# Optimization experiments

Hardware: AMD Instinct MI355X
Metric: run time of the kernel (lower is better)

Reference implementation:

```python
import jax, jax.numpy as jnp
import numpy as np

EMB = 1024
HEADS = 16
HEAD_DIM = EMB // HEADS
B, S = 2, 2048
FF = 4 * EMB
EPS = 1e-5


def setup_inputs() -> dict:
    key = jax.random.key(0)
    ks = jax.random.split(key, 16)
    sc = 0.02
    return {
        "x": jax.random.normal(ks[0], (B, S, EMB), dtype=jnp.float32),
        "ln1_scale": jnp.ones((EMB,), jnp.float32),
        "ln1_shift": jnp.zeros((EMB,), jnp.float32),
        "ln2_scale": jnp.ones((EMB,), jnp.float32),
        "ln2_shift": jnp.zeros((EMB,), jnp.float32),
        "wq": jax.random.normal(ks[1], (EMB, EMB), jnp.float32) * sc,
        "bq": jnp.zeros((EMB,), jnp.float32),
        "wk": jax.random.normal(ks[2], (EMB, EMB), jnp.float32) * sc,
        "bk": jnp.zeros((EMB,), jnp.float32),
        "wv": jax.random.normal(ks[3], (EMB, EMB), jnp.float32) * sc,
        "bv": jnp.zeros((EMB,), jnp.float32),
        "wo": jax.random.normal(ks[4], (EMB, EMB), jnp.float32) * sc,
        "bo": jnp.zeros((EMB,), jnp.float32),
        "w_fc": jax.random.normal(ks[5], (EMB, FF), jnp.float32) * sc,
        "b_fc": jnp.zeros((FF,), jnp.float32),
        "w_proj": jax.random.normal(ks[6], (FF, EMB), jnp.float32) * sc,
        "b_proj": jnp.zeros((EMB,), jnp.float32),
    }


def _layernorm(x, scale, shift):
    # Faithful to source: unbiased std (ddof=1) and eps added to std, not var.
    mean = jnp.mean(x, axis=-1, keepdims=True)
    std = jnp.std(x, axis=-1, keepdims=True, ddof=1)
    return scale * ((x - mean) / (std + EPS)) + shift


def _gelu(x):
    c = jnp.sqrt(jnp.asarray(2.0 / np.pi, x.dtype))
    return 0.5 * x * (1.0 + jnp.tanh(c * (x + 0.044715 * x * x * x)))


def _attention(x, wq, bq, wk, bk, wv, bv, wo, bo):
    b, s, _ = x.shape
    q = (x @ wq + bq).reshape(b, s, HEADS, HEAD_DIM).transpose(0, 2, 1, 3)
    k = (x @ wk + bk).reshape(b, s, HEADS, HEAD_DIM).transpose(0, 2, 1, 3)
    v = (x @ wv + bv).reshape(b, s, HEADS, HEAD_DIM).transpose(0, 2, 1, 3)
    scores = jnp.einsum("bhqd,bhkd->bhqk", q, k)  # [B,H,S,S]
    causal = jnp.triu(jnp.ones((s, s), bool), k=1)
    scores = jnp.where(causal, -jnp.inf, scores)
    attn = jax.nn.softmax(scores / jnp.sqrt(jnp.asarray(HEAD_DIM, x.dtype)), axis=-1)
    ctx = jnp.einsum("bhqk,bhkd->bhqd", attn, v)
    ctx = ctx.transpose(0, 2, 1, 3).reshape(b, s, EMB)
    return ctx @ wo + bo


def reference(x, ln1_scale, ln1_shift, ln2_scale, ln2_shift,
              wq, bq, wk, bk, wv, bv, wo, bo,
              w_fc, b_fc, w_proj, b_proj):
    h = x + _attention(_layernorm(x, ln1_scale, ln1_shift), wq, bq, wk, bk, wv, bv, wo, bo)
    m = _layernorm(h, ln2_scale, ln2_shift)
    m = _gelu(m @ w_fc + b_fc) @ w_proj + b_proj
    return h + m
```

## Files before the change

kernel.cpp:

```cpp
#include <hip/hip_runtime.h>
#include <hip/hip_bf16.h>

typedef float f32x4 __attribute__((ext_vector_type(4)));
typedef __bf16 bf16x8 __attribute__((ext_vector_type(8)));

#define EMB 1024
#define FFD 4096
#define NHEAD 16
#define HD 64
#define SEQ 2048
#define MROWS 4096

__device__ __forceinline__ unsigned short f2bf(float f) {
    unsigned int x = __builtin_bit_cast(unsigned int, f);
    x += 0x7fffu + ((x >> 16) & 1u);
    return (unsigned short)(x >> 16);
}

__device__ __forceinline__ unsigned int pack2bf(float a, float b) {
    return (unsigned int)f2bf(a) | ((unsigned int)f2bf(b) << 16);
}

__device__ __forceinline__ f32x4 mfma16(bf16x8 a, bf16x8 b, f32x4 c) {
    return __builtin_amdgcn_mfma_f32_16x16x32_bf16(a, b, c, 0, 0, 0);
}

__device__ __forceinline__ bf16x8 scale8(bf16x8 v, float s) {
    bf16x8 o;
#pragma unroll
    for (int i = 0; i < 8; ++i) o[i] = (__bf16)((float)v[i] * s);
    return o;
}

__device__ __forceinline__ float gelu_f(float x) {
    float u = 0.7978845608028654f * (x + 0.044715f * x * x * x);
    float e = __expf(2.0f * u);
    float th = 1.0f - 2.0f / (e + 1.0f);
    return 0.5f * x * (1.0f + th);
}

__device__ __forceinline__ void xcd_remap(int& bx, int& by) {
    const int nbx = gridDim.x;
    int id = blockIdx.x + nbx * blockIdx.y;
    int xcd = id & 7, i = id >> 3;
    by = (i / nbx) * 8 + xcd;
    bx = i % nbx;
}

template <int EPI>
__global__ __launch_bounds__(256) void gemm_bt(
    const unsigned short* __restrict__ A, const unsigned short* __restrict__ Bt,
    const float* __restrict__ bias,
    void* __restrict__ outp, int M, int N, int K)
{
    __shared__ unsigned short As[2][128 * 32];
    __shared__ unsigned short Bs[2][128 * 32];
    const int tid  = threadIdx.x;
    const int lane = tid & 63;
    const int wid  = tid >> 6;
    int bx, by; xcd_remap(bx, by);
    const int brow = by << 7;
    const int bcol = bx << 7;
    const int wr = wid >> 1, wc = wid & 1;

    f32x4 acc[4][4];
    const f32x4 zero = {0.f, 0.f, 0.f, 0.f};
#pragma unroll
    for (int m = 0; m < 4; ++m)
#pragma unroll
        for (int n = 0; n < 4; ++n) acc[m][n] = zero;

    const int nk = K >> 5;

    auto stage = [&](int buf, int k0) {
#pragma unroll
        for (int c = 0; c < 2; ++c) {
            int idx = (wid << 10) + (c << 9) + (lane << 3);
            int row = idx >> 5;
            int c8s = (idx >> 3) & 3;
            int c8g = c8s ^ ((row >> 1) & 3);
            const unsigned short* ga = A  + (size_t)(brow + row) * K + k0 + (c8g << 3);
            const unsigned short* gb = Bt + (size_t)(bcol + row) * K + k0 + (c8g << 3);
            __builtin_amdgcn_global_load_lds(
                (const __attribute__((address_space(1))) unsigned int*)ga,
                (__attribute__((address_space(3))) unsigned int*)&As[buf][idx], 16, 0, 0);
            __builtin_amdgcn_global_load_lds(
                (const __attribute__((address_space(1))) unsigned int*)gb,
                (__attribute__((address_space(3))) unsigned int*)&Bs[buf][idx], 16, 0, 0);
        }
    };

    stage(0, 0);
    for (int kt = 0; kt < nk; ++kt) {
        __syncthreads();
        if (kt + 1 < nk) stage((kt + 1) & 1, (kt + 1) << 5);
        const unsigned short* as = As[kt & 1];
        const unsigned short* bs = Bs[kt & 1];
        const int kg = lane >> 4;
        bf16x8 afr[4], bfr[4];
#pragma unroll
        for (int m = 0; m < 4; ++m) {
            int row = (wr << 6) + (m << 4) + (lane & 15);
            int c8  = kg ^ ((row >> 1) & 3);
            afr[m] = *(const bf16x8*)&as[(row << 5) + (c8 << 3)];
        }
#pragma unroll
        for (int n = 0; n < 4; ++n) {
            int row = (wc << 6) + (n << 4) + (lane & 15);
            int c8  = kg ^ ((row >> 1) & 3);
            bfr[n] = *(const bf16x8*)&bs[(row << 5) + (c8 << 3)];
        }
#pragma unroll
        for (int m = 0; m < 4; ++m)
#pragma unroll
            for (int n = 0; n < 4; ++n)
                acc[m][n] = mfma16(afr[m], bfr[n], acc[m][n]);
        __syncthreads();
    }

#pragma unroll
    for (int m = 0; m < 4; ++m) {
#pragma unroll
        for (int n = 0; n < 4; ++n) {
            const int col = bcol + (wc << 6) + (n << 4) + (lane & 15);
            const float bv = bias[col];
#pragma unroll
            for (int r = 0; r < 4; ++r) {
                const int row = brow + (wr << 6) + (m << 4) + ((lane >> 4) << 2) + r;
                float v = acc[m][n][r] + bv;
                if (EPI == 1) v = gelu_f(v);
                ((unsigned short*)outp)[(size_t)row * N + col] = f2bf(v);
            }
        }
    }
}

__global__ __launch_bounds__(256) void gemm_bt_n64(
    const unsigned short* __restrict__ A, const unsigned short* __restrict__ Bt,
    const float* __restrict__ bias, const float* __restrict__ resid,
    float* __restrict__ outp, int M, int N, int K)
{
    __shared__ unsigned short As[2][128 * 64];
    __shared__ unsigned short Bs[2][64 * 64];
    const int tid  = threadIdx.x;
    const int lane = tid & 63;
    const int wid  = tid >> 6;
    int bx, by; xcd_remap(bx, by);
    const int brow = by << 7;
    const int bcol = bx << 6;

    f32x4 acc[2][4];
    const f32x4 zero = {0.f, 0.f, 0.f, 0.f};
#pragma unroll
    for (int m = 0; m < 2; ++m)
#pragma unroll
        for (int n = 0; n < 4; ++n) acc[m][n] = zero;

    const int nk = K >> 6;

    auto stage = [&](int buf, int k0) {
#pragma unroll
        for (int c = 0; c < 4; ++c) {
            int idx = (c << 11) + (tid << 3);
            int row = idx >> 6;
            int c8g = ((idx >> 3) & 7) ^ (row & 7);
            const unsigned short* ga = A + (size_t)(brow + row) * K + k0 + (c8g << 3);
            __builtin_amdgcn_global_load_lds(
                (const __attribute__((address_space(1))) unsigned int*)ga,
                (__attribute__((address_space(3))) unsigned int*)&As[buf][idx], 16, 0, 0);
        }
#pragma unroll
        for (int c = 0; c < 2; ++c) {
            int idx = (c << 11) + (tid << 3);
            int row = idx >> 6;
            int c8g = ((idx >> 3) & 7) ^ (row & 7);
            const unsigned short* gb = Bt + (size_t)(bcol + row) * K + k0 + (c8g << 3);
            __builtin_amdgcn_global_load_lds(
                (const __attribute__((address_space(1))) unsigned int*)gb,
                (__attribute__((address_space(3))) unsigned int*)&Bs[buf][idx], 16, 0, 0);
        }
    };

    stage(0, 0);
    for (int kt = 0; kt < nk; ++kt) {
        __syncthreads();
        if (kt + 1 < nk) stage((kt + 1) & 1, (kt + 1) << 6);
        const unsigned short* as = As[kt & 1];
        const unsigned short* bs = Bs[kt & 1];
        const int kg = lane >> 4;
#pragma unroll
        for (int f = 0; f < 2; ++f) {
            bf16x8 afr[2], bfr[4];
#pragma unroll
            for (int m = 0; m < 2; ++m) {
                int row = (wid << 5) + (m << 4) + (lane & 15);
                int c8  = ((f << 2) + kg) ^ (row & 7);
                afr[m] = *(const bf16x8*)&as[(row << 6) + (c8 << 3)];
            }
#pragma unroll
            for (int n = 0; n < 4; ++n) {
                int row = (n << 4) + (lane & 15);
                int c8  = ((f << 2) + kg) ^ (row & 7);
                bfr[n] = *(const bf16x8*)&bs[(row << 6) + (c8 << 3)];
            }
#pragma unroll
            for (int m = 0; m < 2; ++m)
#pragma unroll
                for (int n = 0; n < 4; ++n)
                    acc[m][n] = mfma16(afr[m], bfr[n], acc[m][n]);
        }
        __syncthreads();
    }

#pragma unroll
    for (int m = 0; m < 2; ++m)
#pragma unroll
        for (int n = 0; n < 4; ++n) {
            const int col = bcol + (n << 4) + (lane & 15);
            const float bv = bias[col];
#pragma unroll
            for (int r = 0; r < 4; ++r) {
                const int row = brow + (wid << 5) + (m << 4) + ((lane >> 4) << 2) + r;
                outp[(size_t)row * N + col] =
                    acc[m][n][r] + bv + resid[(size_t)row * N + col];
            }
        }
}

__global__ __launch_bounds__(256) void layernorm_k(
    const float* __restrict__ x, const float* __restrict__ sc,
    const float* __restrict__ sh, unsigned short* __restrict__ outp)
{
    const int row = blockIdx.x;
    const int tid = threadIdx.x;
    const float4 v = ((const float4*)(x + (size_t)row * EMB))[tid];
    float s  = v.x + v.y + v.z + v.w;
    float ss = v.x * v.x + v.y * v.y + v.z * v.z + v.w * v.w;
#pragma unroll
    for (int o = 32; o > 0; o >>= 1) {
        s  += __shfl_down(s, o);
        ss += __shfl_down(ss, o);
    }
    __shared__ float red[8];
    if ((tid & 63) == 0) { red[tid >> 6] = s; red[(tid >> 6) + 4] = ss; }
    __syncthreads();
    s  = red[0] + red[1] + red[2] + red[3];
    ss = red[4] + red[5] + red[6] + red[7];
    const float mean = s * (1.0f / EMB);
    const float var  = (ss - s * mean) * (1.0f / (EMB - 1));
    const float inv  = 1.0f / (sqrtf(var) + 1e-5f);
    const int c = tid << 2;
    ushort4 o4;
    o4.x = f2bf((v.x - mean) * inv * sc[c + 0] + sh[c + 0]);
    o4.y = f2bf((v.y - mean) * inv * sc[c + 1] + sh[c + 1]);
    o4.z = f2bf((v.z - mean) * inv * sc[c + 2] + sh[c + 2]);
    o4.w = f2bf((v.w - mean) * inv * sc[c + 3] + sh[c + 3]);
    ((ushort4*)(outp + (size_t)row * EMB))[tid] = o4;
}

__global__ __launch_bounds__(256) void vtrans_k(
    const unsigned short* __restrict__ qkv, unsigned short* __restrict__ vt)
{
    __shared__ unsigned short T[64 * 64];
    const int tid = threadIdx.x;
    const int st = blockIdx.x, h = blockIdx.y, b = blockIdx.z;
    const size_t rowbase = (size_t)b * SEQ;
    const unsigned short* vsrc = qkv + (rowbase + (st << 6)) * 3072 + 2 * EMB + h * 64;
#pragma unroll
    for (int it = 0; it < 2; ++it) {
        const int s  = (it << 5) + (tid >> 3);
        const int d8 = tid & 7;
        uint4 w = *(const uint4*)(vsrc + (size_t)s * 3072 + (d8 << 3));
        *(uint4*)&T[(s << 6) + ((d8 ^ (s & 7)) << 3)] = w;
    }
    __syncthreads();
    unsigned short* vdst = vt + ((size_t)(b * NHEAD + h) << 6) * SEQ + (st << 6);
#pragma unroll
    for (int it = 0; it < 2; ++it) {
        const int d  = (it << 5) + (tid >> 3);
        const int s8 = tid & 7;
        unsigned short o8[8];
#pragma unroll
        for (int j = 0; j < 8; ++j) {
            const int s = (s8 << 3) + j;
            o8[j] = T[(s << 6) + (((d >> 3) ^ (s & 7)) << 3) + (d & 7)];
        }
        *(uint4*)(vdst + (size_t)d * SEQ + (s8 << 3)) = *(const uint4*)o8;
    }
}

__global__ __launch_bounds__(256) void attn_k(
    const unsigned short* __restrict__ qkv, const unsigned short* __restrict__ vt,
    unsigned short* __restrict__ ctx)
{
    __shared__ unsigned short Ks[2][64 * 64];
    __shared__ unsigned short Vts[2][64 * 64];
    __shared__ unsigned short Ps[4][16 * 64];
    const int tid  = threadIdx.x;
    const int lane = tid & 63;
    const int wid  = tid >> 6;
    const int q    = lane & 15;
    const int lg   = lane >> 4;

    const int id = blockIdx.x;
    const int xcd = id & 7, i = id >> 3;
    const int grp = ((i >> 4) << 3) + xcd;
    const int pairi = i & 15;
    const int h = grp & 15;
    const int b = grp >> 4;

    const size_t rowbase = (size_t)b * SEQ;
    const unsigned short* kbase = qkv + rowbase * 3072 + EMB + h * 64;
    const unsigned short* vbase = vt + ((size_t)(b * NHEAD + h) << 6) * SEQ;

    auto stage = [&](int buf, int t) {
#pragma unroll
        for (int c = 0; c < 2; ++c) {
            const int idx = (wid << 10) + (c << 9) + (lane << 3);
            {
                const int kv  = idx >> 6;
                const int d8s = ((idx >> 3) & 7) ^ (kv & 7);
                const unsigned short* g = kbase + (size_t)((t << 6) + kv) * 3072 + (d8s << 3);
                __builtin_amdgcn_global_load_lds(
                    (const __attribute__((address_space(1))) unsigned int*)g,
                    (__attribute__((address_space(3))) unsigned int*)&Ks[buf][idx], 16, 0, 0);
            }
            {
                const int d   = idx >> 6;
                const int s8s = ((idx >> 3) & 7) ^ (d & 7);
                const unsigned short* g = vbase + (size_t)d * SEQ + (t << 6) + (s8s << 3);
                __builtin_amdgcn_global_load_lds(
                    (const __attribute__((address_space(1))) unsigned int*)g,
                    (__attribute__((address_space(3))) unsigned int*)&Vts[buf][idx], 16, 0, 0);
            }
        }
    };

    const f32x4 zero = {0.f, 0.f, 0.f, 0.f};
    const float QSC = 0.18033688011112042f;

#pragma unroll 1
    for (int pass = 0; pass < 2; ++pass) {
        const int qt = pass ? (31 - pairi) : pairi;
        const int qrow0 = (qt << 6) + (wid << 4);
        const int qglob = qrow0 + q;

        bf16x8 qf[2];
        {
            const unsigned short* qp = qkv + (rowbase + qglob) * 3072 + h * 64;
            qf[0] = scale8(*(const bf16x8*)&qp[(lg << 3)], QSC);
            qf[1] = scale8(*(const bf16x8*)&qp[32 + (lg << 3)], QSC);
        }

        f32x4 accd[4];
#pragma unroll
        for (int dg = 0; dg < 4; ++dg) accd[dg] = zero;
        float mrow = -__builtin_inff();
        float lrow = 0.f;

        stage(0, 0);
#pragma unroll 1
        for (int t = 0; t <= qt; ++t) {
            __syncthreads();
            if (t < qt) stage((t + 1) & 1, t + 1);
            const unsigned short* ks = Ks[t & 1];
            const unsigned short* vs = Vts[t & 1];

            f32x4 sg[4];
#pragma unroll
            for (int g = 0; g < 4; ++g) {
                f32x4 sv = zero;
#pragma unroll
                for (int f = 0; f < 2; ++f) {
                    const int krow = (g << 4) + q;
                    const int cb   = (f << 5) + (lg << 3);
                    bf16x8 kf = *(const bf16x8*)&ks[(krow << 6) + (cb ^ ((krow & 7) << 3))];
                    sv = mfma16(kf, qf[f], sv);
                }
                sg[g] = sv;
            }
            if (t == qt) {
#pragma unroll
                for (int g = 0; g < 4; ++g) {
#pragma unroll
                    for (int r = 0; r < 4; ++r) {
                        const int kvg = (t << 6) + (g << 4) + (lg << 2) + r;
                        if (kvg > qglob) sg[g][r] = -__builtin_inff();
                    }
                }
            }

            float mx = sg[0][0];
#pragma unroll
            for (int g = 0; g < 4; ++g)
#pragma unroll
                for (int r = 0; r < 4; ++r) mx = fmaxf(mx, sg[g][r]);
            mx = fmaxf(mx, __shfl_xor(mx, 16));
            mx = fmaxf(mx, __shfl_xor(mx, 32));
            if (__any(mx > mrow + 8.0f)) {
                const float mn = fmaxf(mrow, mx);
                const float so = exp2f(mrow - mn);
                mrow = mn;
                lrow *= so;
#pragma unroll
                for (int dg = 0; dg < 4; ++dg) accd[dg] *= so;
            }
            float rs = 0.f;
#pragma unroll
            for (int g = 0; g < 4; ++g)
#pragma unroll
                for (int r = 0; r < 4; ++r) {
                    const float pv = exp2f(sg[g][r] - mrow);
                    sg[g][r] = pv;
                    rs += pv;
                }
            rs += __shfl_xor(rs, 16);
            rs += __shfl_xor(rs, 32);
            lrow += rs;

#pragma unroll
            for (int g = 0; g < 4; ++g) {
                uint2 w;
                w.x = pack2bf(sg[g][0], sg[g][1]);
                w.y = pack2bf(sg[g][2], sg[g][3]);
                const int e = ((g << 4) + (lg << 2)) ^ ((q & 7) << 3);
                *(uint2*)&Ps[wid][(q << 6) + e] = w;
            }

            bf16x8 pa[2];
#pragma unroll
            for (int f = 0; f < 2; ++f) {
                const int e = ((f << 5) + (lg << 3)) ^ ((q & 7) << 3);
                pa[f] = *(const bf16x8*)&Ps[wid][(q << 6) + e];
            }
#pragma unroll
            for (int dg = 0; dg < 4; ++dg) {
#pragma unroll
                for (int f = 0; f < 2; ++f) {
                    const int vrow = (dg << 4) + q;
                    const int cb   = (f << 5) + (lg << 3);
                    bf16x8 vb = *(const bf16x8*)&vs[(vrow << 6) + (cb ^ ((vrow & 7) << 3))];
                    accd[dg] = mfma16(vb, pa[f], accd[dg]);
                }
            }
        }

        const float inv = 1.0f / lrow;
        unsigned short* cp = ctx + (rowbase + qglob) * EMB + h * 64 + (lg << 2);
#pragma unroll
        for (int dg = 0; dg < 4; ++dg) {
            uint2 w;
            w.x = pack2bf(accd[dg][0] * inv, accd[dg][1] * inv);
            w.y = pack2bf(accd[dg][2] * inv, accd[dg][3] * inv);
            *(uint2*)(cp + (dg << 4)) = w;
        }
        __syncthreads();
    }
}

__global__ __launch_bounds__(256) void transpose_cvt(
    const float* __restrict__ W, unsigned short* __restrict__ Wt, int K, int N)
{
    __shared__ float tbuf[32][33];
    const int n0 = blockIdx.x << 5;
    const int k0 = blockIdx.y << 5;
    const int tx = threadIdx.x & 31;
    const int ty = threadIdx.x >> 5;
#pragma unroll
    for (int j = 0; j < 32; j += 8)
        tbuf[ty + j][tx] = W[(size_t)(k0 + ty + j) * N + n0 + tx];
    __syncthreads();
#pragma unroll
    for (int j = 0; j < 32; j += 8)
        Wt[(size_t)(n0 + ty + j) * K + k0 + tx] = f2bf(tbuf[tx][ty + j]);
}

__global__ void pack_bias(const float* __restrict__ bq, const float* __restrict__ bk,
                          const float* __restrict__ bv, float* __restrict__ o)
{
    const int i = blockIdx.x * 256 + threadIdx.x;
    o[i] = (i < 1024) ? bq[i] : (i < 2048) ? bk[i - 1024] : bv[i - 2048];
}

extern "C" void kernel_launch(void* const* d_in, const int* in_sizes, int n_in,
                              void* d_out, int out_size, void* d_ws, size_t ws_size,
                              hipStream_t stream)
{
    const float* x   = (const float*)d_in[0];
    const float* l1s = (const float*)d_in[1];
    const float* l1b = (const float*)d_in[2];
    const float* l2s = (const float*)d_in[3];
    const float* l2b = (const float*)d_in[4];
    const float* wq  = (const float*)d_in[5];
    const float* bq  = (const float*)d_in[6];
    const float* wk  = (const float*)d_in[7];
    const float* bk  = (const float*)d_in[8];
    const float* wv  = (const float*)d_in[9];
    const float* bv  = (const float*)d_in[10];
    const float* wo  = (const float*)d_in[11];
    const float* bo  = (const float*)d_in[12];
    const float* wfc = (const float*)d_in[13];
    const float* bfc = (const float*)d_in[14];
    const float* wpr = (const float*)d_in[15];
    const float* bpr = (const float*)d_in[16];

    unsigned short* WtQKV = (unsigned short*)d_ws;
    unsigned short* WtO   = WtQKV + (size_t)3072 * 1024;
    unsigned short* WtFC  = WtO   + (size_t)1024 * 1024;
    unsigned short* WtPR  = WtFC  + (size_t)4096 * 1024;
    unsigned short* LN1   = WtPR  + (size_t)1024 * 4096;
    unsigned short* QKV   = LN1   + (size_t)4096 * 1024;
    unsigned short* CTX   = QKV   + (size_t)4096 * 3072;
    unsigned short* LN2   = CTX   + (size_t)4096 * 1024;
    unsigned short* Gb    = LN2   + (size_t)4096 * 1024;
    float* H    = (float*)(Gb + (size_t)4096 * 4096);
    float* BQKV = H + (size_t)4096 * 1024;
    unsigned short* VT = Gb;

    dim3 blk(256);
    transpose_cvt<<<dim3(32, 32), blk, 0, stream>>>(wq, WtQKV, 1024, 1024);
    transpose_cvt<<<dim3(32, 32), blk, 0, stream>>>(wk, WtQKV + (size_t)1024 * 1024, 1024, 1024);
    transpose_cvt<<<dim3(32, 32), blk, 0, stream>>>(wv, WtQKV + (size_t)2048 * 1024, 1024, 1024);
    transpose_cvt<<<dim3(32, 32), blk, 0, stream>>>(wo, WtO, 1024, 1024);
    transpose_cvt<<<dim3(128, 32), blk, 0, stream>>>(wfc, WtFC, 1024, 4096);
    transpose_cvt<<<dim3(32, 128), blk, 0, stream>>>(wpr, WtPR, 4096, 1024);
    pack_bias<<<dim3(12), blk, 0, stream>>>(bq, bk, bv, BQKV);

    layernorm_k<<<dim3(4096), blk, 0, stream>>>(x, l1s, l1b, LN1);
    gemm_bt<0><<<dim3(24, 32), blk, 0, stream>>>(LN1, WtQKV, BQKV, QKV, 4096, 3072, 1024);
    vtrans_k<<<dim3(32, NHEAD, 2), blk, 0, stream>>>(QKV, VT);
    attn_k<<<dim3(512), blk, 0, stream>>>(QKV, VT, CTX);
    gemm_bt_n64<<<dim3(16, 32), blk, 0, stream>>>(CTX, WtO, bo, x, H, 4096, 1024, 1024);
    layernorm_k<<<dim3(4096), blk, 0, stream>>>(H, l2s, l2b, LN2);
    gemm_bt<1><<<dim3(32, 32), blk, 0, stream>>>(LN2, WtFC, bfc, Gb, 4096, 4096, 1024);
    gemm_bt_n64<<<dim3(16, 32), blk, 0, stream>>>(Gb, WtPR, bpr, H, (float*)d_out, 4096, 1024, 4096);
}
```

Before: 376.7 us.

## Fold softmax scale into Q weights, add MFMA priority hints, use native bf16 conversion

```diff
diff --git a/kernel.cpp b/kernel.cpp
--- a/kernel.cpp
+++ b/kernel.cpp
@@ -12,24 +12,17 @@
 #define MROWS 4096
 
 __device__ __forceinline__ unsigned short f2bf(float f) {
-    unsigned int x = __builtin_bit_cast(unsigned int, f);
-    x += 0x7fffu + ((x >> 16) & 1u);
-    return (unsigned short)(x >> 16);
+    return __builtin_bit_cast(unsigned short, (__bf16)f);
 }
 
 __device__ __forceinline__ unsigned int pack2bf(float a, float b) {
-    return (unsigned int)f2bf(a) | ((unsigned int)f2bf(b) << 16);
+    unsigned short lo = __builtin_bit_cast(unsigned short, (__bf16)a);
+    unsigned short hi = __builtin_bit_cast(unsigned short, (__bf16)b);
+    return (unsigned int)lo | ((unsigned int)hi << 16);
 }
 
 __device__ __forceinline__ f32x4 mfma16(bf16x8 a, bf16x8 b, f32x4 c) {
     return __builtin_amdgcn_mfma_f32_16x16x32_bf16(a, b, c, 0, 0, 0);
-}
-
-__device__ __forceinline__ bf16x8 scale8(bf16x8 v, float s) {
-    bf16x8 o;
-#pragma unroll
-    for (int i = 0; i < 8; ++i) o[i] = (__bf16)((float)v[i] * s);
-    return o;
 }
 
 __device__ __forceinline__ float gelu_f(float x) {
@@ -110,11 +103,13 @@
             int c8  = kg ^ ((row >> 1) & 3);
             bfr[n] = *(const bf16x8*)&bs[(row << 5) + (c8 << 3)];
         }
+        __builtin_amdgcn_s_setprio(1);
 #pragma unroll
         for (int m = 0; m < 4; ++m)
 #pragma unroll
             for (int n = 0; n < 4; ++n)
                 acc[m][n] = mfma16(afr[m], bfr[n], acc[m][n]);
+        __builtin_amdgcn_s_setprio(0);
         __syncthreads();
     }
 
@@ -203,11 +198,13 @@
                 int c8  = ((f << 2) + kg) ^ (row & 7);
                 bfr[n] = *(const bf16x8*)&bs[(row << 6) + (c8 << 3)];
             }
+            __builtin_amdgcn_s_setprio(1);
 #pragma unroll
             for (int m = 0; m < 2; ++m)
 #pragma unroll
                 for (int n = 0; n < 4; ++n)
                     acc[m][n] = mfma16(afr[m], bfr[n], acc[m][n]);
+            __builtin_amdgcn_s_setprio(0);
         }
         __syncthreads();
     }
@@ -250,11 +247,12 @@
     const float var  = (ss - s * mean) * (1.0f / (EMB - 1));
     const float inv  = 1.0f / (sqrtf(var) + 1e-5f);
     const int c = tid << 2;
-    ushort4 o4;
-    o4.x = f2bf((v.x - mean) * inv * sc[c + 0] + sh[c + 0]);
-    o4.y = f2bf((v.y - mean) * inv * sc[c + 1] + sh[c + 1]);
-    o4.z = f2bf((v.z - mean) * inv * sc[c + 2] + sh[c + 2]);
-    o4.w = f2bf((v.w - mean) * inv * sc[c + 3] + sh[c + 3]);
+    ushort2 o01, o23;
+    o01.x = f2bf((v.x - mean) * inv * sc[c + 0] + sh[c + 0]);
+    o01.y = f2bf((v.y - mean) * inv * sc[c + 1] + sh[c + 1]);
+    o23.x = f2bf((v.z - mean) * inv * sc[c + 2] + sh[c + 2]);
+    o23.y = f2bf((v.w - mean) * inv * sc[c + 3] + sh[c + 3]);
+    ushort4 o4 = {o01.x, o01.y, o23.x, o23.y};
     ((ushort4*)(outp + (size_t)row * EMB))[tid] = o4;
 }
 
@@ -337,7 +335,6 @@
     };
 
     const f32x4 zero = {0.f, 0.f, 0.f, 0.f};
-    const float QSC = 0.18033688011112042f;
 
 #pragma unroll 1
     for (int pass = 0; pass < 2; ++pass) {
@@ -348,8 +345,8 @@
         bf16x8 qf[2];
         {
             const unsigned short* qp = qkv + (rowbase + qglob) * 3072 + h * 64;
-            qf[0] = scale8(*(const bf16x8*)&qp[(lg << 3)], QSC);
-            qf[1] = scale8(*(const bf16x8*)&qp[32 + (lg << 3)], QSC);
+            qf[0] = *(const bf16x8*)&qp[(lg << 3)];
+            qf[1] = *(const bf16x8*)&qp[32 + (lg << 3)];
         }
 
         f32x4 accd[4];
@@ -367,6 +364,7 @@
             const unsigned short* vs = Vts[t & 1];
 
             f32x4 sg[4];
+            __builtin_amdgcn_s_setprio(1);
 #pragma unroll
             for (int g = 0; g < 4; ++g) {
                 f32x4 sv = zero;
@@ -379,6 +377,7 @@
                 }
                 sg[g] = sv;
             }
+            __builtin_amdgcn_s_setprio(0);
             if (t == qt) {
 #pragma unroll
                 for (int g = 0; g < 4; ++g) {
@@ -390,11 +389,11 @@
                 }
             }
 
-            float mx = sg[0][0];
+            float mg[4];
 #pragma unroll
             for (int g = 0; g < 4; ++g)
-#pragma unroll
-                for (int r = 0; r < 4; ++r) mx = fmaxf(mx, sg[g][r]);
+                mg[g] = fmaxf(fmaxf(sg[g][0], sg[g][1]), fmaxf(sg[g][2], sg[g][3]));
+            float mx = fmaxf(fmaxf(mg[0], mg[1]), fmaxf(mg[2], mg[3]));
             mx = fmaxf(mx, __shfl_xor(mx, 16));
             mx = fmaxf(mx, __shfl_xor(mx, 32));
             if (__any(mx > mrow + 8.0f)) {
@@ -433,6 +432,7 @@
                 const int e = ((f << 5) + (lg << 3)) ^ ((q & 7) << 3);
                 pa[f] = *(const bf16x8*)&Ps[wid][(q << 6) + e];
             }
+            __builtin_amdgcn_s_setprio(1);
 #pragma unroll
             for (int dg = 0; dg < 4; ++dg) {
 #pragma unroll
@@ -443,6 +443,7 @@
                     accd[dg] = mfma16(vb, pa[f], accd[dg]);
                 }
             }
+            __builtin_amdgcn_s_setprio(0);
         }
 
         const float inv = 1.0f / lrow;
@@ -459,7 +460,8 @@
 }
 
 __global__ __launch_bounds__(256) void transpose_cvt(
-    const float* __restrict__ W, unsigned short* __restrict__ Wt, int K, int N)
+    const float* __restrict__ W, unsigned short* __restrict__ Wt, int K, int N,
+    float scale)
 {
     __shared__ float tbuf[32][33];
     const int n0 = blockIdx.x << 5;
@@ -468,7 +470,7 @@
     const int ty = threadIdx.x >> 5;
 #pragma unroll
     for (int j = 0; j < 32; j += 8)
-        tbuf[ty + j][tx] = W[(size_t)(k0 + ty + j) * N + n0 + tx];
+        tbuf[ty + j][tx] = W[(size_t)(k0 + ty + j) * N + n0 + tx] * scale;
     __syncthreads();
 #pragma unroll
     for (int j = 0; j < 32; j += 8)
@@ -476,10 +478,11 @@
 }
 
 __global__ void pack_bias(const float* __restrict__ bq, const float* __restrict__ bk,
-                          const float* __restrict__ bv, float* __restrict__ o)
+                          const float* __restrict__ bv, float* __restrict__ o,
+                          float qsc)
 {
     const int i = blockIdx.x * 256 + threadIdx.x;
-    o[i] = (i < 1024) ? bq[i] : (i < 2048) ? bk[i - 1024] : bv[i - 2048];
+    o[i] = (i < 1024) ? bq[i] * qsc : (i < 2048) ? bk[i - 1024] : bv[i - 2048];
 }
 
 extern "C" void kernel_launch(void* const* d_in, const int* in_sizes, int n_in,
@@ -504,6 +507,8 @@
     const float* wpr = (const float*)d_in[15];
     const float* bpr = (const float*)d_in[16];
 
+    const float QSC = 0.18033688011112042f;
+
     unsigned short* WtQKV = (unsigned short*)d_ws;
     unsigned short* WtO   = WtQKV + (size_t)3072 * 1024;
     unsigned short* WtFC  = WtO   + (size_t)1024 * 1024;
@@ -518,13 +523,13 @@
     unsigned short* VT = Gb;
 
     dim3 blk(256);
-    transpose_cvt<<<dim3(32, 32), blk, 0, stream>>>(wq, WtQKV, 1024, 1024);
-    transpose_cvt<<<dim3(32, 32), blk, 0, stream>>>(wk, WtQKV + (size_t)1024 * 1024, 1024, 1024);
-    transpose_cvt<<<dim3(32, 32), blk, 0, stream>>>(wv, WtQKV + (size_t)2048 * 1024, 1024, 1024);
-    transpose_cvt<<<dim3(32, 32), blk, 0, stream>>>(wo, WtO, 1024, 1024);
-    transpose_cvt<<<dim3(128, 32), blk, 0, stream>>>(wfc, WtFC, 1024, 4096);
-    transpose_cvt<<<dim3(32, 128), blk, 0, stream>>>(wpr, WtPR, 4096, 1024);
-    pack_bias<<<dim3(12), blk, 0, stream>>>(bq, bk, bv, BQKV);
+    transpose_cvt<<<dim3(32, 32), blk, 0, stream>>>(wq, WtQKV, 1024, 1024, QSC);
+    transpose_cvt<<<dim3(32, 32), blk, 0, stream>>>(wk, WtQKV + (size_t)1024 * 1024, 1024, 1024, 1.0f);
+    transpose_cvt<<<dim3(32, 32), blk, 0, stream>>>(wv, WtQKV + (size_t)2048 * 1024, 1024, 1024, 1.0f);
+    transpose_cvt<<<dim3(32, 32), blk, 0, stream>>>(wo, WtO, 1024, 1024, 1.0f);
+    transpose_cvt<<<dim3(128, 32), blk, 0, stream>>>(wfc, WtFC, 1024, 4096, 1.0f);
+    transpose_cvt<<<dim3(32, 128), blk, 0, stream>>>(wpr, WtPR, 4096, 1024, 1.0f);
+    pack_bias<<<dim3(12), blk, 0, stream>>>(bq, bk, bv, BQKV, QSC);
 
     layernorm_k<<<dim3(4096), blk, 0, stream>>>(x, l1s, l1b, LN1);
     gemm_bt<0><<<dim3(24, 32), blk, 0, stream>>>(LN1, WtQKV, BQKV, QKV, 4096, 3072, 1024);
```

New measurement: 375.0 us. Within noise of the previous version (-0.5%).
